# Performance work log

Hardware: AMD Instinct MI355X
Metric: run time of the kernel (lower is better)

The kernel has to match this reference:

```python
import jax, jax.numpy as jnp
import numpy as np

N_NODES = 100000
N_EDGES = 1600000
N_GRAPHS = 512
IN_DIM, HID_DIM, OUT_DIM = 128, 256, 128
EPS = 0.0  # PyG GINConv default eps (train_eps=False)


def setup_inputs() -> dict:
    key = jax.random.key(0)
    ks = jax.random.split(key, 9)
    x = jax.random.normal(ks[0], (N_NODES, IN_DIM), dtype=jnp.float32)
    edge_index = jax.random.randint(ks[1], (2, N_EDGES), 0, N_NODES, dtype=jnp.int64)
    batch_ids = jnp.sort(jax.random.randint(ks[2], (N_NODES,), 0, N_GRAPHS, dtype=jnp.int64))
    s1 = 1.0 / np.sqrt(IN_DIM)
    s2 = 1.0 / np.sqrt(HID_DIM)
    W1 = jax.random.normal(ks[3], (IN_DIM, HID_DIM), dtype=jnp.float32) * s1
    b1 = jax.random.normal(ks[4], (HID_DIM,), dtype=jnp.float32) * s1
    W2 = jax.random.normal(ks[5], (HID_DIM, HID_DIM), dtype=jnp.float32) * s2
    b2 = jax.random.normal(ks[6], (HID_DIM,), dtype=jnp.float32) * s2
    Wo = jax.random.normal(ks[7], (HID_DIM, OUT_DIM), dtype=jnp.float32) * s2
    bo = jax.random.normal(ks[8], (OUT_DIM,), dtype=jnp.float32) * s2
    return {"x": x, "edge_index": edge_index, "batch_ids": batch_ids,
            "W1": W1, "b1": b1, "W2": W2, "b2": b2, "Wo": Wo, "bo": bo}


def reference(x, edge_index, batch_ids, W1, b1, W2, b2, Wo, bo):
    src, dst = edge_index[0], edge_index[1]
    # GIN aggregation: sum of neighbor features scattered to destination nodes
    agg = jax.ops.segment_sum(x[src], dst, num_segments=N_NODES)  # [N, in]
    h = (1.0 + EPS) * x + agg
    # GIN MLP: Linear -> ReLU -> Linear -> ReLU
    h = jax.nn.relu(h @ W1 + b1)
    h = jax.nn.relu(h @ W2 + b2)
    out = h @ Wo + bo  # output_layer
    # global_add_pool over graphs
    pooled = jax.ops.segment_sum(out, batch_ids, num_segments=N_GRAPHS)  # [G, out]
    return pooled
```

## Files before the change

### kernel.cpp

```cpp
#include <hip/hip_runtime.h>

#define N_NODES  100000
#define M_PAD    100096
#define N_EDGES  1600000
#define N_GRAPHS 512
#define IN_DIM   128
#define HID_DIM  256
#define OUT_DIM  128

#define NB       782
#define BCAP     3072
#define CHUNK    2048
#define BKB      ((N_EDGES + CHUNK - 1) / CHUNK)

typedef __bf16 bf16x8 __attribute__((ext_vector_type(8)));
typedef __bf16 bf16x4 __attribute__((ext_vector_type(4)));
typedef __bf16 bf16x2 __attribute__((ext_vector_type(2)));
typedef float  f32x4  __attribute__((ext_vector_type(4)));

#define WP_L2_BASE 32768
#define WP_L3_BASE 98304
#define WP_TOTAL   131072

#define R_X    (N_NODES * IN_DIM / 4)
#define R_APAD ((M_PAD - N_NODES) * IN_DIM / 4)
#define R_WP   WP_TOTAL
#define R_OUT  (N_GRAPHS * OUT_DIM / 4)
#define R_CUR  NB
#define R_TOTAL (R_X + R_APAD + R_WP + R_OUT + R_CUR)

__global__ __launch_bounds__(256) void init_kernel(const float* __restrict__ x,
                                                   const float* __restrict__ W1,
                                                   const float* __restrict__ W2,
                                                   const float* __restrict__ Wo,
                                                   __bf16* __restrict__ xb,
                                                   __bf16* __restrict__ Apad,
                                                   __bf16* __restrict__ Wp,
                                                   float* __restrict__ outbuf,
                                                   int* __restrict__ gcursor) {
    long long i = (long long)blockIdx.x * blockDim.x + threadIdx.x;
    if (i < R_X) {
        float4 v = ((const float4*)x)[i];
        bf16x4 h;
        h.x = (__bf16)v.x; h.y = (__bf16)v.y; h.z = (__bf16)v.z; h.w = (__bf16)v.w;
        ((bf16x4*)xb)[i] = h;
        return;
    }
    i -= R_X;
    if (i < R_APAD) {
        bf16x4 z; z.x = (__bf16)0.f; z.y = (__bf16)0.f; z.z = (__bf16)0.f; z.w = (__bf16)0.f;
        ((bf16x4*)Apad)[i] = z;
        return;
    }
    i -= R_APAD;
    if (i < R_WP) {
        int idx = (int)i;
        const float* src;
        int K, Nn, base;
        if (idx < WP_L2_BASE)      { src = W1; K = 128; Nn = 256; base = 0; }
        else if (idx < WP_L3_BASE) { src = W2; K = 256; Nn = 256; base = WP_L2_BASE; }
        else                       { src = Wo; K = 256; Nn = 128; base = WP_L3_BASE; }
        int r0 = idx - base;
        int slabElems = 32 * K;
        int j = r0 / slabElems;
        int r = r0 % slabElems;
        int KS = K / 32;
        int p = r >> 9;
        int lane = (r >> 3) & 63;
        int e = r & 7;
        int s = p % KS, t = p / KS;
        int quad = lane >> 4, l16 = lane & 15;
        int n = j * 32 + t * 16 + l16;
        int k = s * 32 + quad * 8 + e;
        Wp[idx] = (__bf16)src[(size_t)k * Nn + n];
        return;
    }
    i -= R_WP;
    if (i < R_OUT) {
        ((float4*)outbuf)[i] = make_float4(0.f, 0.f, 0.f, 0.f);
        return;
    }
    i -= R_OUT;
    if (i < R_CUR) gcursor[i] = 0;
}

__global__ __launch_bounds__(256) void bucket_v2_kernel(const int* __restrict__ ei,
                                                        int* __restrict__ gcursor,
                                                        unsigned* __restrict__ pairBuf) {
    __shared__ int lcnt[NB];
    __shared__ int lbase[NB];
    const int tid = threadIdx.x;
    const int e0 = blockIdx.x * CHUNK;

    for (int b = tid; b < NB; b += 256) lcnt[b] = 0;
    __syncthreads();

    for (int i = tid; i < CHUNK; i += 256) {
        int e = e0 + i;
        if (e < N_EDGES) atomicAdd(&lcnt[ei[N_EDGES + e] >> 7], 1);
    }
    __syncthreads();

    for (int b = tid; b < NB; b += 256) {
        int c = lcnt[b];
        lbase[b] = c ? atomicAdd(&gcursor[b], c) : 0;
        lcnt[b] = 0;
    }
    __syncthreads();

    for (int i = tid; i < CHUNK; i += 256) {
        int e = e0 + i;
        if (e < N_EDGES) {
            int s = ei[e];
            int d = ei[N_EDGES + e];
            int b = d >> 7;
            int pos = lbase[b] + atomicAdd(&lcnt[b], 1);
            if (pos < BCAP)
                pairBuf[(size_t)b * BCAP + pos] = (unsigned)s | ((unsigned)(d & 127) << 17);
        }
    }
}

__global__ __launch_bounds__(256) void passB_kernel(const unsigned* __restrict__ pairBuf,
                                                    const int* __restrict__ gcursor,
                                                    int* __restrict__ nbr,
                                                    int* __restrict__ offsets,
                                                    int* __restrict__ deg) {
    __shared__ int lcnt[128];
    __shared__ int loffs[128];
    __shared__ int lcur[128];
    const int b = blockIdx.x;
    const int tid = threadIdx.x;
    const int node0 = b << 7;
    const int cnt = min(gcursor[b], BCAP);
    const int base = b * BCAP;
    const unsigned* pb = pairBuf + (size_t)b * BCAP;

    if (tid < 128) { lcnt[tid] = 0; lcur[tid] = 0; }
    __syncthreads();

    for (int i = tid; i < cnt; i += 256)
        atomicAdd(&lcnt[pb[i] >> 17], 1);
    __syncthreads();

    if (tid < 128) loffs[tid] = lcnt[tid];
    __syncthreads();
    for (int st = 1; st < 128; st <<= 1) {
        int add = (tid < 128 && tid >= st) ? loffs[tid - st] : 0;
        __syncthreads();
        if (tid < 128) loffs[tid] += add;
        __syncthreads();
    }
    int excl = 0;
    if (tid < 128) {
        excl = loffs[tid] - lcnt[tid];
        int node = node0 + tid;
        if (node < N_NODES) {
            deg[node] = lcnt[tid];
            offsets[node] = base + excl;
        }
    }
    __syncthreads();
    if (tid < 128) loffs[tid] = excl;
    __syncthreads();

    for (int i = tid; i < cnt; i += 256) {
        unsigned u = pb[i];
        int dl = u >> 17;
        int slot = atomicAdd(&lcur[dl], 1);
        nbr[base + loffs[dl] + slot] = (int)(u & 0x1FFFF);
    }
}

__global__ __launch_bounds__(256) void aggregate_kernel(const __bf16* __restrict__ xb,
                                                        const int* __restrict__ offsets,
                                                        const int* __restrict__ deg,
                                                        const int* __restrict__ nbr,
                                                        __bf16* __restrict__ A) {
    int v = blockIdx.x * 4 + (threadIdx.x >> 6);
    v = __builtin_amdgcn_readfirstlane(v);
    int lane = threadIdx.x & 63;
    if (v >= N_NODES) return;
    int off = offsets[v];
    int len = deg[v];
    const int c0 = lane * 2;
    bf16x2 self = *(const bf16x2*)(xb + (size_t)v * IN_DIM + c0);
    float ax = (float)self.x, ay = (float)self.y;

    int addr = off + lane;
    if (addr > NB * BCAP - 1) addr = NB * BCAP - 1;
    int myidx = nbr[addr];

    int lim = len < 64 ? len : 64;
    int j = 0;
    for (; j + 8 <= lim; j += 8) {
        int s0 = __shfl(myidx, j + 0, 64);
        int s1 = __shfl(myidx, j + 1, 64);
        int s2 = __shfl(myidx, j + 2, 64);
        int s3 = __shfl(myidx, j + 3, 64);
        int s4 = __shfl(myidx, j + 4, 64);
        int s5 = __shfl(myidx, j + 5, 64);
        int s6 = __shfl(myidx, j + 6, 64);
        int s7 = __shfl(myidx, j + 7, 64);
        bf16x2 v0 = *(const bf16x2*)(xb + (size_t)s0 * IN_DIM + c0);
        bf16x2 v1 = *(const bf16x2*)(xb + (size_t)s1 * IN_DIM + c0);
        bf16x2 v2 = *(const bf16x2*)(xb + (size_t)s2 * IN_DIM + c0);
        bf16x2 v3 = *(const bf16x2*)(xb + (size_t)s3 * IN_DIM + c0);
        bf16x2 v4 = *(const bf16x2*)(xb + (size_t)s4 * IN_DIM + c0);
        bf16x2 v5 = *(const bf16x2*)(xb + (size_t)s5 * IN_DIM + c0);
        bf16x2 v6 = *(const bf16x2*)(xb + (size_t)s6 * IN_DIM + c0);
        bf16x2 v7 = *(const bf16x2*)(xb + (size_t)s7 * IN_DIM + c0);
        ax += (float)v0.x + (float)v1.x + (float)v2.x + (float)v3.x
            + (float)v4.x + (float)v5.x + (float)v6.x + (float)v7.x;
        ay += (float)v0.y + (float)v1.y + (float)v2.y + (float)v3.y
            + (float)v4.y + (float)v5.y + (float)v6.y + (float)v7.y;
    }
    for (; j < lim; ++j) {
        int s = __shfl(myidx, j, 64);
        bf16x2 vv = *(const bf16x2*)(xb + (size_t)s * IN_DIM + c0);
        ax += (float)vv.x;
        ay += (float)vv.y;
    }
    for (; j < len; ++j) {
        int s = nbr[off + j];
        bf16x2 vv = *(const bf16x2*)(xb + (size_t)s * IN_DIM + c0);
        ax += (float)vv.x;
        ay += (float)vv.y;
    }
    bf16x2 h;
    h.x = (__bf16)ax;
    h.y = (__bf16)ay;
    *(bf16x2*)(A + (size_t)v * IN_DIM + c0) = h;
}

__device__ __forceinline__ void load_group_p(const __bf16* __restrict__ p, int lane,
                                             bf16x8* __restrict__ dst) {
    #pragma unroll
    for (int e = 0; e < 8; ++e)
        dst[e] = *(const bf16x8*)(p + (e * 64 + lane) * 8);
}

__device__ __forceinline__ void store_H(__bf16* __restrict__ H, int j, int quad, int l16,
                                        const f32x4 (&acc)[2][2], float bt0, float bt1) {
    const int c7 = l16 & 7;
    const int ch = l16 >> 3;
    #pragma unroll
    for (int i = 0; i < 2; ++i)
        #pragma unroll
        for (int t = 0; t < 2; ++t) {
            const float bb = t ? bt1 : bt0;
            #pragma unroll
            for (int rr = 0; rr < 4; ++rr) {
                int row = i * 16 + quad * 4 + rr;
                int cidx = (j * 4 + t * 2 + ch + row) & 31;
                float v = fmaxf(acc[i][t][rr] + bb, 0.f);
                H[row * 256 + cidx * 8 + c7] = (__bf16)v;
            }
        }
}

__global__ __launch_bounds__(64) void mlp_fused(const __bf16* __restrict__ A,
                                                const __bf16* __restrict__ Wp,
                                                const float* __restrict__ b1,
                                                const float* __restrict__ b2,
                                                const float* __restrict__ bo,
                                                float* __restrict__ out,
                                                const int* __restrict__ batch) {
    __shared__ __bf16 H[32 * 256];

    const int lane = threadIdx.x;
    const int quad = lane >> 4, l16 = lane & 15;
    const size_t mblk = (size_t)blockIdx.x * 32;
    const int r0g = (int)mblk;
    int gfirst = (r0g < N_NODES) ? batch[r0g] : -2;
    int glast  = (r0g + 31 < N_NODES) ? batch[r0g + 31] : -1;

    bf16x8 a[2][8];
    bf16x8 buf0[8];
    bf16x8 buf1[8];

    const __bf16* wp = Wp;
    load_group_p(wp, lane, buf0);

    #pragma unroll
    for (int i = 0; i < 2; ++i)
        #pragma unroll
        for (int s = 0; s < 4; ++s)
            a[i][s] = *(const bf16x8*)(A + (mblk + i * 16 + l16) * IN_DIM + s * 32 + quad * 8);

    #pragma unroll 1
    for (int j = 0; j < 8; j += 2) {
        {
            load_group_p(wp + 4096, lane, buf1);
            float bt0 = b1[j * 32 + l16];
            float bt1 = b1[j * 32 + 16 + l16];
            f32x4 acc[2][2] = {};
            #pragma unroll
            for (int p = 0; p < 8; ++p) {
                const int t = p >> 2, s = p & 3;
                acc[0][t] = __builtin_amdgcn_mfma_f32_16x16x32_bf16(a[0][s], buf0[p], acc[0][t], 0, 0, 0);
                acc[1][t] = __builtin_amdgcn_mfma_f32_16x16x32_bf16(a[1][s], buf0[p], acc[1][t], 0, 0, 0);
            }
            store_H(H, j, quad, l16, acc, bt0, bt1);
        }
        {
            load_group_p(wp + 8192, lane, buf0);
            float bt0 = b1[(j + 1) * 32 + l16];
            float bt1 = b1[(j + 1) * 32 + 16 + l16];
            f32x4 acc[2][2] = {};
            #pragma unroll
            for (int p = 0; p < 8; ++p) {
                const int t = p >> 2, s = p & 3;
                acc[0][t] = __builtin_amdgcn_mfma_f32_16x16x32_bf16(a[0][s], buf1[p], acc[0][t], 0, 0, 0);
                acc[1][t] = __builtin_amdgcn_mfma_f32_16x16x32_bf16(a[1][s], buf1[p], acc[1][t], 0, 0, 0);
            }
            store_H(H, j + 1, quad, l16, acc, bt0, bt1);
        }
        wp += 8192;
    }
    __syncthreads();

    #pragma unroll
    for (int i = 0; i < 2; ++i)
        #pragma unroll
        for (int s = 0; s < 8; ++s) {
            int row = i * 16 + l16;
            a[i][s] = *(const bf16x8*)(H + row * 256 + (((s * 4 + quad) + row) & 31) * 8);
        }
    __syncthreads();

    #pragma unroll 1
    for (int j = 0; j < 8; ++j) {
        load_group_p(wp + 4096, lane, buf1);
        float bt0 = b2[j * 32 + l16];
        float bt1 = b2[j * 32 + 16 + l16];
        f32x4 acc[2][2] = {};
        #pragma unroll
        for (int p = 0; p < 8; ++p) {
            acc[0][0] = __builtin_amdgcn_mfma_f32_16x16x32_bf16(a[0][p], buf0[p], acc[0][0], 0, 0, 0);
            acc[1][0] = __builtin_amdgcn_mfma_f32_16x16x32_bf16(a[1][p], buf0[p], acc[1][0], 0, 0, 0);
        }
        load_group_p(wp + 8192, lane, buf0);
        #pragma unroll
        for (int p = 0; p < 8; ++p) {
            acc[0][1] = __builtin_amdgcn_mfma_f32_16x16x32_bf16(a[0][p], buf1[p], acc[0][1], 0, 0, 0);
            acc[1][1] = __builtin_amdgcn_mfma_f32_16x16x32_bf16(a[1][p], buf1[p], acc[1][1], 0, 0, 0);
        }
        store_H(H, j, quad, l16, acc, bt0, bt1);
        wp += 8192;
    }
    __syncthreads();

    #pragma unroll
    for (int i = 0; i < 2; ++i)
        #pragma unroll
        for (int s = 0; s < 8; ++s) {
            int row = i * 16 + l16;
            a[i][s] = *(const bf16x8*)(H + row * 256 + (((s * 4 + quad) + row) & 31) * 8);
        }

    #pragma unroll 1
    for (int j = 0; j < 4; ++j) {
        load_group_p(wp + 4096, lane, buf1);
        float bt0 = bo[j * 32 + l16];
        float bt1 = bo[j * 32 + 16 + l16];
        f32x4 acc[2][2] = {};
        #pragma unroll
        for (int p = 0; p < 8; ++p) {
            acc[0][0] = __builtin_amdgcn_mfma_f32_16x16x32_bf16(a[0][p], buf0[p], acc[0][0], 0, 0, 0);
            acc[1][0] = __builtin_amdgcn_mfma_f32_16x16x32_bf16(a[1][p], buf0[p], acc[1][0], 0, 0, 0);
        }
        load_group_p(wp + 8192, lane, buf0);
        #pragma unroll
        for (int p = 0; p < 8; ++p) {
            acc[0][1] = __builtin_amdgcn_mfma_f32_16x16x32_bf16(a[0][p], buf1[p], acc[0][1], 0, 0, 0);
            acc[1][1] = __builtin_amdgcn_mfma_f32_16x16x32_bf16(a[1][p], buf1[p], acc[1][1], 0, 0, 0);
        }

        if (gfirst == glast) {
            #pragma unroll
            for (int t = 0; t < 2; ++t) {
                float sum = 0.f;
                #pragma unroll
                for (int i = 0; i < 2; ++i)
                    #pragma unroll
                    for (int rr = 0; rr < 4; ++rr) sum += acc[i][t][rr];
                sum += __shfl_xor(sum, 16, 64);
                sum += __shfl_xor(sum, 32, 64);
                if (quad == 0) {
                    int c = j * 32 + t * 16 + l16;
                    float bb = t ? bt1 : bt0;
                    atomicAdd(out + (size_t)gfirst * OUT_DIM + c, sum + 32.f * bb);
                }
            }
        } else {
            #pragma unroll
            for (int i = 0; i < 2; ++i)
                #pragma unroll
                for (int rr = 0; rr < 4; ++rr) {
                    int m = r0g + i * 16 + quad * 4 + rr;
                    if (m < N_NODES) {
                        int g = batch[m];
                        #pragma unroll
                        for (int t = 0; t < 2; ++t) {
                            int c = j * 32 + t * 16 + l16;
                            float bb = t ? bt1 : bt0;
                            atomicAdd(out + (size_t)g * OUT_DIM + c, acc[i][t][rr] + bb);
                        }
                    }
                }
        }
        wp += 8192;
    }
}

extern "C" void kernel_launch(void* const* d_in, const int* in_sizes, int n_in,
                              void* d_out, int out_size, void* d_ws, size_t ws_size,
                              hipStream_t stream) {
    const float* x  = (const float*)d_in[0];
    const int*   ei = (const int*)d_in[1];
    const int*   bi = (const int*)d_in[2];
    const float* W1 = (const float*)d_in[3];
    const float* b1 = (const float*)d_in[4];
    const float* W2 = (const float*)d_in[5];
    const float* b2 = (const float*)d_in[6];
    const float* Wo = (const float*)d_in[7];
    const float* bo = (const float*)d_in[8];
    float* out = (float*)d_out;

    __bf16* A  = (__bf16*)d_ws;
    __bf16* xb = A + (size_t)M_PAD * IN_DIM;
    __bf16* Wp = xb + (size_t)N_NODES * IN_DIM;
    unsigned* pairBuf = (unsigned*)(Wp + WP_TOTAL);
    int* nbr      = (int*)(pairBuf + (size_t)NB * BCAP);
    int* offsets  = nbr + (size_t)NB * BCAP;
    int* deg      = offsets + N_NODES;
    int* gcursor  = deg + N_NODES;

    init_kernel<<<(R_TOTAL + 255) / 256, 256, 0, stream>>>(
        x, W1, W2, Wo, xb, A + (size_t)N_NODES * IN_DIM, Wp, out, gcursor);

    bucket_v2_kernel<<<BKB, 256, 0, stream>>>(ei, gcursor, pairBuf);
    passB_kernel<<<NB, 256, 0, stream>>>(pairBuf, gcursor, nbr, offsets, deg);

    aggregate_kernel<<<(N_NODES + 3) / 4, 256, 0, stream>>>(xb, offsets, deg, nbr, A);

    mlp_fused<<<M_PAD / 32, 64, 0, stream>>>(A, Wp, b1, b2, bo, out, bi);
}
```

Measured before the change: 290.0 us.

## Fuse CSR build and neighbor aggregation into one kernel using shared-memory sort

Merges the per-bucket counting-sort pass and the aggregation kernel into a single kernel. Each 512-thread block sorts its 128-node bucket's edges into LDS, then its 8 waves aggregate neighbor features straight from the LDS index list. This removes the global nbr/offsets/deg arrays, their write and read traffic, and one kernel launch. The cost is only 782 blocks doing the gather work, which may lower occupancy and latency hiding compared with the previous 25k-block aggregation launch.

```diff
diff --git a/kernel.cpp b/kernel.cpp
--- a/kernel.cpp
+++ b/kernel.cpp
@@ -121,25 +121,28 @@
     }
 }
 
-__global__ __launch_bounds__(256) void passB_kernel(const unsigned* __restrict__ pairBuf,
-                                                    const int* __restrict__ gcursor,
-                                                    int* __restrict__ nbr,
-                                                    int* __restrict__ offsets,
-                                                    int* __restrict__ deg) {
+#define AGG_THREADS 512
+
+__global__ __launch_bounds__(AGG_THREADS) void aggB_kernel(const unsigned* __restrict__ pairBuf,
+                                                           const int* __restrict__ gcursor,
+                                                           const __bf16* __restrict__ xb,
+                                                           __bf16* __restrict__ A) {
     __shared__ int lcnt[128];
     __shared__ int loffs[128];
     __shared__ int lcur[128];
+    __shared__ int offx[128];
+    __shared__ unsigned sorted[BCAP];
+
     const int b = blockIdx.x;
     const int tid = threadIdx.x;
     const int node0 = b << 7;
     const int cnt = min(gcursor[b], BCAP);
-    const int base = b * BCAP;
     const unsigned* pb = pairBuf + (size_t)b * BCAP;
 
     if (tid < 128) { lcnt[tid] = 0; lcur[tid] = 0; }
     __syncthreads();
 
-    for (int i = tid; i < cnt; i += 256)
+    for (int i = tid; i < cnt; i += AGG_THREADS)
         atomicAdd(&lcnt[pb[i] >> 17], 1);
     __syncthreads();
 
@@ -151,86 +154,75 @@
         if (tid < 128) loffs[tid] += add;
         __syncthreads();
     }
-    int excl = 0;
-    if (tid < 128) {
-        excl = loffs[tid] - lcnt[tid];
-        int node = node0 + tid;
-        if (node < N_NODES) {
-            deg[node] = lcnt[tid];
-            offsets[node] = base + excl;
-        }
-    }
-    __syncthreads();
-    if (tid < 128) loffs[tid] = excl;
-    __syncthreads();
-
-    for (int i = tid; i < cnt; i += 256) {
+    if (tid < 128) offx[tid] = loffs[tid] - lcnt[tid];
+    __syncthreads();
+
+    for (int i = tid; i < cnt; i += AGG_THREADS) {
         unsigned u = pb[i];
         int dl = u >> 17;
         int slot = atomicAdd(&lcur[dl], 1);
-        nbr[base + loffs[dl] + slot] = (int)(u & 0x1FFFF);
-    }
-}
-
-__global__ __launch_bounds__(256) void aggregate_kernel(const __bf16* __restrict__ xb,
-                                                        const int* __restrict__ offsets,
-                                                        const int* __restrict__ deg,
-                                                        const int* __restrict__ nbr,
-                                                        __bf16* __restrict__ A) {
-    int v = blockIdx.x * 4 + (threadIdx.x >> 6);
-    v = __builtin_amdgcn_readfirstlane(v);
-    int lane = threadIdx.x & 63;
-    if (v >= N_NODES) return;
-    int off = offsets[v];
-    int len = deg[v];
+        sorted[offx[dl] + slot] = u & 0x1FFFF;
+    }
+    __syncthreads();
+
+    const int wid = tid >> 6;
+    const int lane = tid & 63;
     const int c0 = lane * 2;
-    bf16x2 self = *(const bf16x2*)(xb + (size_t)v * IN_DIM + c0);
-    float ax = (float)self.x, ay = (float)self.y;
-
-    int addr = off + lane;
-    if (addr > NB * BCAP - 1) addr = NB * BCAP - 1;
-    int myidx = nbr[addr];
-
-    int lim = len < 64 ? len : 64;
-    int j = 0;
-    for (; j + 8 <= lim; j += 8) {
-        int s0 = __shfl(myidx, j + 0, 64);
-        int s1 = __shfl(myidx, j + 1, 64);
-        int s2 = __shfl(myidx, j + 2, 64);
-        int s3 = __shfl(myidx, j + 3, 64);
-        int s4 = __shfl(myidx, j + 4, 64);
-        int s5 = __shfl(myidx, j + 5, 64);
-        int s6 = __shfl(myidx, j + 6, 64);
-        int s7 = __shfl(myidx, j + 7, 64);
-        bf16x2 v0 = *(const bf16x2*)(xb + (size_t)s0 * IN_DIM + c0);
-        bf16x2 v1 = *(const bf16x2*)(xb + (size_t)s1 * IN_DIM + c0);
-        bf16x2 v2 = *(const bf16x2*)(xb + (size_t)s2 * IN_DIM + c0);
-        bf16x2 v3 = *(const bf16x2*)(xb + (size_t)s3 * IN_DIM + c0);
-        bf16x2 v4 = *(const bf16x2*)(xb + (size_t)s4 * IN_DIM + c0);
-        bf16x2 v5 = *(const bf16x2*)(xb + (size_t)s5 * IN_DIM + c0);
-        bf16x2 v6 = *(const bf16x2*)(xb + (size_t)s6 * IN_DIM + c0);
-        bf16x2 v7 = *(const bf16x2*)(xb + (size_t)s7 * IN_DIM + c0);
-        ax += (float)v0.x + (float)v1.x + (float)v2.x + (float)v3.x
-            + (float)v4.x + (float)v5.x + (float)v6.x + (float)v7.x;
-        ay += (float)v0.y + (float)v1.y + (float)v2.y + (float)v3.y
-            + (float)v4.y + (float)v5.y + (float)v6.y + (float)v7.y;
-    }
-    for (; j < lim; ++j) {
-        int s = __shfl(myidx, j, 64);
-        bf16x2 vv = *(const bf16x2*)(xb + (size_t)s * IN_DIM + c0);
-        ax += (float)vv.x;
-        ay += (float)vv.y;
-    }
-    for (; j < len; ++j) {
-        int s = nbr[off + j];
-        bf16x2 vv = *(const bf16x2*)(xb + (size_t)s * IN_DIM + c0);
-        ax += (float)vv.x;
-        ay += (float)vv.y;
-    }
-    bf16x2 h;
-    h.x = (__bf16)ax;
-    h.y = (__bf16)ay;
-    *(bf16x2*)(A + (size_t)v * IN_DIM + c0) = h;
+
+    #pragma unroll 1
+    for (int n = wid; n < 128; n += (AGG_THREADS / 64)) {
+        int v = node0 + n;
+        if (v >= N_NODES) break;
+        int off = offx[n];
+        int len = lcnt[n];
+        bf16x2 self = *(const bf16x2*)(xb + (size_t)v * IN_DIM + c0);
+        float ax = (float)self.x, ay = (float)self.y;
+
+        int addr = off + lane;
+        if (addr >= cnt) addr = (cnt > 0) ? cnt - 1 : 0;
+        int myidx = (int)sorted[addr];
+
+        int lim = len < 64 ? len : 64;
+        int j = 0;
+        for (; j + 8 <= lim; j += 8) {
+            int s0 = __shfl(myidx, j + 0, 64);
+            int s1 = __shfl(myidx, j + 1, 64);
+            int s2 = __shfl(myidx, j + 2, 64);
+            int s3 = __shfl(myidx, j + 3, 64);
+            int s4 = __shfl(myidx, j + 4, 64);
+            int s5 = __shfl(myidx, j + 5, 64);
+            int s6 = __shfl(myidx, j + 6, 64);
+            int s7 = __shfl(myidx, j + 7, 64);
+            bf16x2 v0 = *(const bf16x2*)(xb + (size_t)s0 * IN_DIM + c0);
+            bf16x2 v1 = *(const bf16x2*)(xb + (size_t)s1 * IN_DIM + c0);
+            bf16x2 v2 = *(const bf16x2*)(xb + (size_t)s2 * IN_DIM + c0);
+            bf16x2 v3 = *(const bf16x2*)(xb + (size_t)s3 * IN_DIM + c0);
+            bf16x2 v4 = *(const bf16x2*)(xb + (size_t)s4 * IN_DIM + c0);
+            bf16x2 v5 = *(const bf16x2*)(xb + (size_t)s5 * IN_DIM + c0);
+            bf16x2 v6 = *(const bf16x2*)(xb + (size_t)s6 * IN_DIM + c0);
+            bf16x2 v7 = *(const bf16x2*)(xb + (size_t)s7 * IN_DIM + c0);
+            ax += (float)v0.x + (float)v1.x + (float)v2.x + (float)v3.x
+                + (float)v4.x + (float)v5.x + (float)v6.x + (float)v7.x;
+            ay += (float)v0.y + (float)v1.y + (float)v2.y + (float)v3.y
+                + (float)v4.y + (float)v5.y + (float)v6.y + (float)v7.y;
+        }
+        for (; j < lim; ++j) {
+            int s = __shfl(myidx, j, 64);
+            bf16x2 vv = *(const bf16x2*)(xb + (size_t)s * IN_DIM + c0);
+            ax += (float)vv.x;
+            ay += (float)vv.y;
+        }
+        for (; j < len; ++j) {
+            int s = (int)sorted[off + j];
+            bf16x2 vv = *(const bf16x2*)(xb + (size_t)s * IN_DIM + c0);
+            ax += (float)vv.x;
+            ay += (float)vv.y;
+        }
+        bf16x2 h;
+        h.x = (__bf16)ax;
+        h.y = (__bf16)ay;
+        *(bf16x2*)(A + (size_t)v * IN_DIM + c0) = h;
+    }
 }
 
 __device__ __forceinline__ void load_group_p(const __bf16* __restrict__ p, int lane,
@@ -432,18 +424,14 @@
     __bf16* xb = A + (size_t)M_PAD * IN_DIM;
     __bf16* Wp = xb + (size_t)N_NODES * IN_DIM;
     unsigned* pairBuf = (unsigned*)(Wp + WP_TOTAL);
-    int* nbr      = (int*)(pairBuf + (size_t)NB * BCAP);
-    int* offsets  = nbr + (size_t)NB * BCAP;
-    int* deg      = offsets + N_NODES;
-    int* gcursor  = deg + N_NODES;
+    int* gcursor  = (int*)(pairBuf + (size_t)NB * BCAP);
 
     init_kernel<<<(R_TOTAL + 255) / 256, 256, 0, stream>>>(
         x, W1, W2, Wo, xb, A + (size_t)N_NODES * IN_DIM, Wp, out, gcursor);
 
     bucket_v2_kernel<<<BKB, 256, 0, stream>>>(ei, gcursor, pairBuf);
-    passB_kernel<<<NB, 256, 0, stream>>>(pairBuf, gcursor, nbr, offsets, deg);
-
-    aggregate_kernel<<<(N_NODES + 3) / 4, 256, 0, stream>>>(xb, offsets, deg, nbr, A);
+
+    aggB_kernel<<<NB, AGG_THREADS, 0, stream>>>(pairBuf, gcursor, xb, A);
 
     mlp_fused<<<M_PAD / 32, 64, 0, stream>>>(A, Wp, b1, b2, bo, out, bi);
 }
```

Result: no change. 287.6 us (-0.8%).
